# Kernel tuning notes

Hardware: AMD Instinct MI355X
Metric: run time of the kernel (lower is better)

The kernel has to match this reference:

```python
import jax, jax.numpy as jnp
import numpy as np

HEAD_SIZE = 128
N_EMBED = 2048
B, T = 4, 4096


def setup_inputs() -> dict:
    key = jax.random.key(0)
    kx, kq, kk, kv = jax.random.split(key, 4)
    s = 1.0 / np.sqrt(N_EMBED)
    return {
        "x": jax.random.normal(kx, (B, T, N_EMBED), dtype=jnp.float32),
        "Wq": jax.random.normal(kq, (N_EMBED, HEAD_SIZE), dtype=jnp.float32) * s,
        "Wk": jax.random.normal(kk, (N_EMBED, HEAD_SIZE), dtype=jnp.float32) * s,
        "Wv": jax.random.normal(kv, (N_EMBED, HEAD_SIZE), dtype=jnp.float32) * s,
    }


def reference(x, Wq, Wk, Wv):
    # x: [B, T, C]; projections (no bias)
    q = jnp.einsum('btc,cd->btd', x, Wq)  # [B, T, D]
    k = jnp.einsum('btc,cd->btd', x, Wk)
    v = jnp.einsum('btc,cd->btd', x, Wv)
    scale = q.shape[-1] ** -0.5
    scores = jnp.einsum('btd,bsd->bts', q, k) * scale  # [B, T, T]
    T_ = x.shape[1]
    causal = jnp.tril(jnp.ones((T_, T_), dtype=bool))
    scores = jnp.where(causal, scores, -jnp.inf)
    weight = jax.nn.softmax(scores, axis=-1)
    # dropout is identity in eval mode
    out = jnp.einsum('bts,bsd->btd', weight, v)  # [B, T, D]
    return out
```

## Files before the change

kernel.cpp:

```cpp
#include <hip/hip_runtime.h>
#include <hip/hip_bf16.h>
#include <stdint.h>

typedef unsigned short ushort_t;
typedef short v8s __attribute__((ext_vector_type(8)));
typedef float f32x4 __attribute__((ext_vector_type(4)));
typedef float f32x16 __attribute__((ext_vector_type(16)));

#define MFMA16(a, b, c) __builtin_amdgcn_mfma_f32_16x16x32_bf16(a, b, c, 0, 0, 0)
#define MFMA32(a, b, c) __builtin_amdgcn_mfma_f32_32x32x16_bf16(a, b, c, 0, 0, 0)

typedef __attribute__((address_space(1))) void gvoid;
typedef __attribute__((address_space(3))) void svoid;

__device__ __forceinline__ void gld16(const void* g, void* s) {
    __builtin_amdgcn_global_load_lds((gvoid*)g, (svoid*)s, 16, 0, 0);
}

__device__ __forceinline__ ushort_t f2bf(float f) {
    union { __hip_bfloat16 b; ushort_t u; } c;
    c.b = __float2bfloat16(f);
    return c.u;
}

__device__ __forceinline__ unsigned f2bf2(float a, float b) {
    union { __hip_bfloat162 b2; unsigned u; } c;
    c.b2 = __float22bfloat162_rn(make_float2(a, b));
    return c.u;
}

__global__ void transpose_w(const float* __restrict__ Wq, const float* __restrict__ Wk,
                            const float* __restrict__ Wv, ushort_t* __restrict__ WT) {
    __shared__ float tile[64][132];
    int bid = blockIdx.x;
    int w = bid >> 5;
    int k0 = (bid & 31) << 6;
    const float* W = (w == 0) ? Wq : ((w == 1) ? Wk : Wv);
    int tid = threadIdx.x;
    #pragma unroll
    for (int i = 0; i < 8; i++) {
        int row = i * 8 + (tid >> 5);
        int col = (tid & 31) * 4;
        float4 v = *(const float4*)(W + (size_t)(k0 + row) * 128 + col);
        tile[row][col] = v.x; tile[row][col + 1] = v.y;
        tile[row][col + 2] = v.z; tile[row][col + 3] = v.w;
    }
    __syncthreads();
    int n = tid >> 1, kh = (tid & 1) * 32;
    ushort_t* dst = WT + ((size_t)(w * 128 + n)) * 2048 + k0 + kh;
    #pragma unroll
    for (int j = 0; j < 32; j += 4) {
        union { ushort_t u[4]; uint2 v2; } pk;
        #pragma unroll
        for (int e = 0; e < 4; e++) pk.u[e] = f2bf(tile[kh + j + e][n]);
        *(uint2*)(dst + j) = pk.v2;
    }
}

#define PROJ_CVT_WRITE(RS, CUR)                                               \
    {                                                                         \
        union { unsigned u[4]; v8s v; } p0, p1;                               \
        p0.u[0] = f2bf2(RS[0][0], RS[0][1]); p0.u[1] = f2bf2(RS[0][2], RS[0][3]); \
        p0.u[2] = f2bf2(RS[1][0], RS[1][1]); p0.u[3] = f2bf2(RS[1][2], RS[1][3]); \
        p1.u[0] = f2bf2(RS[2][0], RS[2][1]); p1.u[1] = f2bf2(RS[2][2], RS[2][3]); \
        p1.u[2] = f2bf2(RS[3][0], RS[3][1]); p1.u[3] = f2bf2(RS[3][2], RS[3][3]); \
        *(v8s*)((char*)abuf + ((CUR) ^ 1) * 8192 + awb0) = p0.v;              \
        *(v8s*)((char*)abuf + ((CUR) ^ 1) * 8192 + awb1) = p1.v;              \
    }

#define PJ_STEP(IT, RLOAD, RCVT, DOX, DOB)                                    \
    {                                                                         \
        const int cur = (IT) & 1;                                             \
        if (DOB) {                                                            \
            _Pragma("unroll")                                                 \
            for (int i = 0; i < 6; i++)                                       \
                gld16(bsrc[i] + (size_t)((IT) + 1) * 128,                     \
                      (char*)bbuf + (cur ^ 1) * 24576 + (wid * 6 + i) * 1024);\
        }                                                                     \
        __builtin_amdgcn_sched_barrier(0);                                    \
        if (DOX) {                                                            \
            _Pragma("unroll")                                                 \
            for (int c = 0; c < 4; c++)                                       \
                RLOAD[c] = *(const f32x4*)(xp + (size_t)((IT) + 2) * 256 + c * 16); \
        }                                                                     \
        __builtin_amdgcn_sched_barrier(0);                                    \
        const char* ab = (const char*)abuf + cur * 8192;                      \
        const char* bb = (const char*)bbuf + cur * 24576;                     \
        _Pragma("unroll")                                                     \
        for (int kk = 0; kk < 2; kk++) {                                      \
            v8s af[4], bf[3];                                                 \
            _Pragma("unroll")                                                 \
            for (int m = 0; m < 4; m++) {                                     \
                int row = m * 16 + lr;                                        \
                af[m] = *(const v8s*)(ab + row * 128 +                        \
                         ((kk * 64 + lg * 16) ^ ((row & 7) << 4)));           \
            }                                                                 \
            _Pragma("unroll")                                                 \
            for (int n = 0; n < 3; n++) {                                     \
                int row = wid * 48 + n * 16 + lr;                             \
                bf[n] = *(const v8s*)(bb + row * 128 +                        \
                         ((kk * 64 + lg * 16) ^ ((row & 7) << 4)));           \
            }                                                                 \
            __builtin_amdgcn_s_setprio(1);                                    \
            _Pragma("unroll")                                                 \
            for (int m = 0; m < 4; m++)                                       \
                _Pragma("unroll")                                             \
                for (int n = 0; n < 3; n++)                                   \
                    acc[m][n] = MFMA16(af[m], bf[n], acc[m][n]);              \
            __builtin_amdgcn_s_setprio(0);                                    \
        }                                                                     \
        if (DOB) PROJ_CVT_WRITE(RCVT, cur);                                   \
        __builtin_amdgcn_sched_barrier(0);                                    \
        if (DOB) {                                                            \
            if (DOX) { asm volatile("s_waitcnt vmcnt(4)" ::: "memory"); }     \
            else     { asm volatile("s_waitcnt vmcnt(0)" ::: "memory"); }     \
            asm volatile("s_waitcnt lgkmcnt(0)" ::: "memory");                \
            __builtin_amdgcn_s_barrier();                                     \
        }                                                                     \
        __builtin_amdgcn_sched_barrier(0);                                    \
    }

__launch_bounds__(256, 2)
__global__ void proj_kernel(const float* __restrict__ x, const ushort_t* __restrict__ WT,
                            ushort_t* __restrict__ q, ushort_t* __restrict__ kb,
                            ushort_t* __restrict__ vb) {
    __shared__ ushort_t abuf[2][4096];
    __shared__ ushort_t bbuf[2][12288];

    int bid = blockIdx.x;
    int mt8 = bid & 7, nh = (bid >> 3) & 1, mg = bid >> 4;
    int mtile = mg * 8 + mt8;
    size_t m0 = (size_t)mtile * 64;
    int c0 = nh * 192;
    int tid = threadIdx.x, lane = tid & 63, wid = tid >> 6;
    int lg = lane >> 4, lr = lane & 15;

    f32x4 acc[4][3];
    #pragma unroll
    for (int m = 0; m < 4; m++)
        #pragma unroll
        for (int n = 0; n < 3; n++) acc[m][n] = (f32x4){0.f, 0.f, 0.f, 0.f};

    int ar = 16 * wid + (lane >> 2);
    const char* xp = (const char*)x + (m0 + ar) * 8192 + (lane & 3) * 64;
    int aswz = (ar & 7) << 4;
    int awb0 = ar * 128 + (((lane & 3) * 32 + 0) ^ aswz);
    int awb1 = ar * 128 + (((lane & 3) * 32 + 16) ^ aswz);

    const char* bsrc[6];
    #pragma unroll
    for (int i = 0; i < 6; i++) {
        int row = 8 * (wid * 6 + i) + (lane >> 3);
        int col = ((lane & 7) * 16) ^ ((row & 7) << 4);
        bsrc[i] = (const char*)WT + (size_t)(c0 + row) * 4096 + col;
    }

    f32x4 s0[4], s1[4];
    #pragma unroll
    for (int i = 0; i < 6; i++)
        gld16(bsrc[i], (char*)bbuf + (wid * 6 + i) * 1024);
    #pragma unroll
    for (int c = 0; c < 4; c++) s0[c] = *(const f32x4*)(xp + c * 16);
    #pragma unroll
    for (int c = 0; c < 4; c++) s1[c] = *(const f32x4*)(xp + 256 + c * 16);
    PROJ_CVT_WRITE(s0, 1);
    asm volatile("s_waitcnt lgkmcnt(0)" ::: "memory");
    __builtin_amdgcn_s_barrier();

    for (int it2 = 0; it2 < 30; it2 += 2) {
        PJ_STEP(it2,     s0, s1, 1, 1);
        PJ_STEP(it2 + 1, s1, s0, 1, 1);
    }
    PJ_STEP(30, s0, s1, 0, 1);
    PJ_STEP(31, s1, s0, 0, 0);

    #pragma unroll
    for (int m = 0; m < 4; m++) {
        #pragma unroll
        for (int e = 0; e < 4; e++) {
            size_t row = m0 + (size_t)(m * 16 + 4 * lg + e);
            int t = (int)(row & 4095);
            size_t base = (row >> 12) * 524288;
            #pragma unroll
            for (int n = 0; n < 3; n++) {
                int col = c0 + wid * 48 + n * 16 + lr;
                int w = col >> 7, d = col & 127;
                ushort_t val = f2bf(acc[m][n][e]);
                if (w == 0)
                    q[base + (size_t)(t >> 5) * 4096 + (d >> 4) * 512 + ((d >> 3) & 1) * 256 + (t & 31) * 8 + (d & 7)] = val;
                else if (w == 1)
                    kb[base + (size_t)(t >> 5) * 4096 + (d >> 4) * 512 + ((d >> 3) & 1) * 256 + (t & 31) * 8 + (d & 7)] = val;
                else
                    vb[base + (size_t)(t >> 4) * 2048 + (d >> 5) * 512 + ((t >> 3) & 1) * 256 + (d & 31) * 8 + (t & 7)] = val;
            }
        }
    }
}

__device__ __forceinline__ f32x16 zero16() {
    f32x16 z;
    #pragma unroll
    for (int i = 0; i < 16; i++) z[i] = 0.f;
    return z;
}

#define ATT_PVC(SV, BASE, VC, CNEXT)                                          \
    {                                                                         \
        unsigned a0 = f2bf2(SV[(BASE) + 0], SV[(BASE) + 1]);                  \
        unsigned a1 = f2bf2(SV[(BASE) + 2], SV[(BASE) + 3]);                  \
        unsigned b0 = f2bf2(SV[(BASE) + 4], SV[(BASE) + 5]);                  \
        unsigned b1 = f2bf2(SV[(BASE) + 6], SV[(BASE) + 7]);                  \
        unsigned snd0 = hi ? a0 : b0, snd1 = hi ? a1 : b1;                    \
        unsigned rcv0 = (unsigned)__shfl_xor((int)snd0, 32);                  \
        unsigned rcv1 = (unsigned)__shfl_xor((int)snd1, 32);                  \
        union { unsigned u[4]; v8s v; } pf;                                   \
        pf.u[0] = hi ? rcv0 : a0;                                             \
        pf.u[1] = hi ? rcv1 : a1;                                             \
        pf.u[2] = hi ? b0 : rcv0;                                             \
        pf.u[3] = hi ? b1 : rcv1;                                             \
        __builtin_amdgcn_s_setprio(1);                                        \
        _Pragma("unroll")                                                     \
        for (int dt = 0; dt < 4; dt++)                                        \
            accO[dt] = MFMA32(VC[dt], pf.v, accO[dt]);                        \
        __builtin_amdgcn_s_setprio(0);                                        \
        if ((CNEXT) >= 0) {                                                   \
            _Pragma("unroll")                                                 \
            for (int dt = 0; dt < 4; dt++)                                    \
                VC[dt] = *(const v8s*)(vg + (CNEXT) * 2048 + dt * 512);       \
        }                                                                     \
    }

__launch_bounds__(256, 2)
__global__ void attn_kernel(const ushort_t* __restrict__ q, const ushort_t* __restrict__ kb,
                            const ushort_t* __restrict__ vb, float* __restrict__ out) {
    __shared__ float obuf[4][4][16][64];
    __shared__ float stat[2][4][64];

    int bid = blockIdx.x;
    int xcd = bid & 7, rk = bid >> 3;
    int b = xcd >> 1;
    int g = rk * 2 + (xcd & 1);
    int qt = (g & 1) ? (g >> 1) : (127 - (g >> 1));
    int qt0 = qt * 32;
    int tid = threadIdx.x, lane = tid & 63, wid = tid >> 6;
    int hi = lane >> 5, lo = lane & 31;
    size_t bb = (size_t)b * 524288;
    int nt = (qt >> 1) + 1;
    const float cexp = 0.08838834764831845f * 1.4426950408889634f;

    v8s qf[8];
    {
        const ushort_t* qg = q + bb + (size_t)qt * 4096 + (size_t)lane * 8;
        #pragma unroll
        for (int ks = 0; ks < 8; ks++) qf[ks] = *(const v8s*)(qg + ks * 512);
    }

    f32x16 accO[4];
    #pragma unroll
    for (int dt = 0; dt < 4; dt++) accO[dt] = zero16();
    float mrun = -1e30f, lrun = 0.f;

    for (int t = wid; t < nt; t += 4) {
        const ushort_t* kg = kb + bb + (size_t)t * 8192 + (size_t)lane * 8;
        const ushort_t* vg = vb + bb + (size_t)t * 8192 + (size_t)lane * 8;

        f32x16 s0 = zero16(), s1 = zero16();
        __builtin_amdgcn_s_setprio(1);
        #pragma unroll
        for (int ks = 0; ks < 8; ks++) {
            v8s kf = *(const v8s*)(kg + ks * 512);
            s0 = MFMA32(kf, qf[ks], s0);
        }
        #pragma unroll
        for (int ks = 0; ks < 8; ks++) {
            v8s kf = *(const v8s*)(kg + 4096 + ks * 512);
            s1 = MFMA32(kf, qf[ks], s1);
        }
        __builtin_amdgcn_s_setprio(0);

        v8s vA[4], vB[4];
        #pragma unroll
        for (int dt = 0; dt < 4; dt++) vA[dt] = *(const v8s*)(vg + dt * 512);
        #pragma unroll
        for (int dt = 0; dt < 4; dt++) vB[dt] = *(const v8s*)(vg + 2048 + dt * 512);

        if (t == nt - 1) {
            int qrow = qt0 + lo;
            #pragma unroll
            for (int r = 0; r < 16; r++) {
                int kvb = t * 64 + (r & 3) + 8 * (r >> 2) + 4 * hi;
                if (kvb > qrow) s0[r] = -1e30f;
                if (kvb + 32 > qrow) s1[r] = -1e30f;
            }
        }

        float mx = s0[0];
        #pragma unroll
        for (int r = 1; r < 16; r++) mx = fmaxf(mx, s0[r]);
        #pragma unroll
        for (int r = 0; r < 16; r++) mx = fmaxf(mx, s1[r]);
        mx = fmaxf(mx, __shfl_xor(mx, 32));

        if (__any(mx > mrun + 62.7f)) {
            float mnew = fmaxf(mrun, mx);
            float fr = exp2f((mrun - mnew) * cexp);
            lrun *= fr;
            #pragma unroll
            for (int dt = 0; dt < 4; dt++)
                #pragma unroll
                for (int r = 0; r < 16; r++) accO[dt][r] *= fr;
            mrun = mnew;
        }
        float mc = mrun * cexp;
        float rs = 0.f;
        #pragma unroll
        for (int r = 0; r < 16; r++) { s0[r] = exp2f(fmaf(s0[r], cexp, -mc)); rs += s0[r]; }
        #pragma unroll
        for (int r = 0; r < 16; r++) { s1[r] = exp2f(fmaf(s1[r], cexp, -mc)); rs += s1[r]; }
        rs += __shfl_xor(rs, 32);
        lrun += rs;

        ATT_PVC(s0, 0, vA, 2);
        ATT_PVC(s0, 8, vB, 3);
        ATT_PVC(s1, 0, vA, -1);
        ATT_PVC(s1, 8, vB, -1);
    }

    #pragma unroll
    for (int dt = 0; dt < 4; dt++)
        #pragma unroll
        for (int r = 0; r < 16; r++)
            obuf[wid][dt][r][lane] = accO[dt][r];
    stat[0][wid][lane] = mrun;
    stat[1][wid][lane] = lrun;
    __syncthreads();

    float m0 = stat[0][0][lane], m1 = stat[0][1][lane];
    float m2 = stat[0][2][lane], m3 = stat[0][3][lane];
    float m = fmaxf(fmaxf(m0, m1), fmaxf(m2, m3));
    float f0 = exp2f((m0 - m) * cexp), f1 = exp2f((m1 - m) * cexp);
    float f2 = exp2f((m2 - m) * cexp), f3 = exp2f((m3 - m) * cexp);
    float lsum = f0 * stat[1][0][lane] + f1 * stat[1][1][lane]
               + f2 * stat[1][2][lane] + f3 * stat[1][3][lane];
    float linv = 1.0f / lsum;

    float o[16];
    #pragma unroll
    for (int r = 0; r < 16; r++)
        o[r] = (f0 * obuf[0][wid][r][lane] + f1 * obuf[1][wid][r][lane]
              + f2 * obuf[2][wid][r][lane] + f3 * obuf[3][wid][r][lane]) * linv;

    float* orow = out + ((size_t)b * 4096 + qt0 + lo) * 128 + wid * 32 + 4 * hi;
    #pragma unroll
    for (int a = 0; a < 4; a++) {
        float4 vv;
        vv.x = o[4 * a + 0]; vv.y = o[4 * a + 1];
        vv.z = o[4 * a + 2]; vv.w = o[4 * a + 3];
        *(float4*)(orow + 8 * a) = vv;
    }
}

extern "C" void kernel_launch(void* const* d_in, const int* in_sizes, int n_in,
                              void* d_out, int out_size, void* d_ws, size_t ws_size,
                              hipStream_t stream) {
    const float* x  = (const float*)d_in[0];
    const float* Wq = (const float*)d_in[1];
    const float* Wk = (const float*)d_in[2];
    const float* Wv = (const float*)d_in[3];
    float* out = (float*)d_out;
    char* ws = (char*)d_ws;

    ushort_t* q  = (ushort_t*)(ws);
    ushort_t* kb = (ushort_t*)(ws + (4u << 20));
    ushort_t* vb = (ushort_t*)(ws + (8u << 20));
    ushort_t* WT = (ushort_t*)(ws + (12u << 20));

    transpose_w<<<dim3(96), dim3(256), 0, stream>>>(Wq, Wk, Wv, WT);
    proj_kernel<<<dim3(512), dim3(256), 0, stream>>>(x, WT, q, kb, vb);
    attn_kernel<<<dim3(512), dim3(256), 0, stream>>>(q, kb, vb, out);
}
```

Before: 98.80 us.

## Retile projection kernel to 64x128 blocks with 2x2 waves and staggered K start

```diff
diff --git a/kernel.cpp b/kernel.cpp
--- a/kernel.cpp
+++ b/kernel.cpp
@@ -57,89 +57,91 @@
     }
 }
 
-#define PROJ_CVT_WRITE(RS, CUR)                                               \
+#define PJ_CVT_WRITE(RS, PAR)                                                 \
     {                                                                         \
         union { unsigned u[4]; v8s v; } p0, p1;                               \
         p0.u[0] = f2bf2(RS[0][0], RS[0][1]); p0.u[1] = f2bf2(RS[0][2], RS[0][3]); \
         p0.u[2] = f2bf2(RS[1][0], RS[1][1]); p0.u[3] = f2bf2(RS[1][2], RS[1][3]); \
         p1.u[0] = f2bf2(RS[2][0], RS[2][1]); p1.u[1] = f2bf2(RS[2][2], RS[2][3]); \
         p1.u[2] = f2bf2(RS[3][0], RS[3][1]); p1.u[3] = f2bf2(RS[3][2], RS[3][3]); \
-        *(v8s*)((char*)abuf + ((CUR) ^ 1) * 8192 + awb0) = p0.v;              \
-        *(v8s*)((char*)abuf + ((CUR) ^ 1) * 8192 + awb1) = p1.v;              \
-    }
-
-#define PJ_STEP(IT, RLOAD, RCVT, DOX, DOB)                                    \
+        *(v8s*)((char*)abuf + (PAR) * 8192 + awb0) = p0.v;                    \
+        *(v8s*)((char*)abuf + (PAR) * 8192 + awb1) = p1.v;                    \
+    }
+
+#define PJ_STEP(PAR, J, RLOAD, RCVT, DOX, DOB)                                \
     {                                                                         \
-        const int cur = (IT) & 1;                                             \
         if (DOB) {                                                            \
-            _Pragma("unroll")                                                 \
-            for (int i = 0; i < 6; i++)                                       \
-                gld16(bsrc[i] + (size_t)((IT) + 1) * 128,                     \
-                      (char*)bbuf + (cur ^ 1) * 24576 + (wid * 6 + i) * 1024);\
+            int itn = (koff + (J) + 1) & 31;                                  \
+            _Pragma("unroll")                                                 \
+            for (int i = 0; i < 4; i++)                                       \
+                gld16(bsrc[i] + (size_t)itn * 128,                            \
+                      (char*)bbuf + ((PAR) ^ 1) * 16384 + (4 * wid + i) * 1024); \
         }                                                                     \
         __builtin_amdgcn_sched_barrier(0);                                    \
         if (DOX) {                                                            \
+            int itx = (koff + (J) + 2) & 31;                                  \
             _Pragma("unroll")                                                 \
             for (int c = 0; c < 4; c++)                                       \
-                RLOAD[c] = *(const f32x4*)(xp + (size_t)((IT) + 2) * 256 + c * 16); \
+                RLOAD[c] = *(const f32x4*)(xp + (size_t)itx * 256 + c * 16);  \
         }                                                                     \
         __builtin_amdgcn_sched_barrier(0);                                    \
-        const char* ab = (const char*)abuf + cur * 8192;                      \
-        const char* bb = (const char*)bbuf + cur * 24576;                     \
+        const char* ab = (const char*)abuf + (PAR) * 8192;                    \
+        const char* bb = (const char*)bbuf + (PAR) * 16384;                   \
         _Pragma("unroll")                                                     \
         for (int kk = 0; kk < 2; kk++) {                                      \
-            v8s af[4], bf[3];                                                 \
-            _Pragma("unroll")                                                 \
-            for (int m = 0; m < 4; m++) {                                     \
-                int row = m * 16 + lr;                                        \
+            v8s af[2], bf[4];                                                 \
+            _Pragma("unroll")                                                 \
+            for (int m = 0; m < 2; m++) {                                     \
+                int row = wr * 32 + m * 16 + lr;                              \
                 af[m] = *(const v8s*)(ab + row * 128 +                        \
                          ((kk * 64 + lg * 16) ^ ((row & 7) << 4)));           \
             }                                                                 \
             _Pragma("unroll")                                                 \
-            for (int n = 0; n < 3; n++) {                                     \
-                int row = wid * 48 + n * 16 + lr;                             \
+            for (int n = 0; n < 4; n++) {                                     \
+                int row = wc * 64 + n * 16 + lr;                              \
                 bf[n] = *(const v8s*)(bb + row * 128 +                        \
                          ((kk * 64 + lg * 16) ^ ((row & 7) << 4)));           \
             }                                                                 \
             __builtin_amdgcn_s_setprio(1);                                    \
             _Pragma("unroll")                                                 \
-            for (int m = 0; m < 4; m++)                                       \
+            for (int m = 0; m < 2; m++)                                       \
                 _Pragma("unroll")                                             \
-                for (int n = 0; n < 3; n++)                                   \
+                for (int n = 0; n < 4; n++)                                   \
                     acc[m][n] = MFMA16(af[m], bf[n], acc[m][n]);              \
             __builtin_amdgcn_s_setprio(0);                                    \
         }                                                                     \
-        if (DOB) PROJ_CVT_WRITE(RCVT, cur);                                   \
-        __builtin_amdgcn_sched_barrier(0);                                    \
         if (DOB) {                                                            \
+            PJ_CVT_WRITE(RCVT, (PAR) ^ 1);                                    \
             if (DOX) { asm volatile("s_waitcnt vmcnt(4)" ::: "memory"); }     \
             else     { asm volatile("s_waitcnt vmcnt(0)" ::: "memory"); }     \
             asm volatile("s_waitcnt lgkmcnt(0)" ::: "memory");                \
             __builtin_amdgcn_s_barrier();                                     \
         }                                                                     \
-        __builtin_amdgcn_sched_barrier(0);                                    \
-    }
-
-__launch_bounds__(256, 2)
+    }
+
+__launch_bounds__(256, 3)
 __global__ void proj_kernel(const float* __restrict__ x, const ushort_t* __restrict__ WT,
                             ushort_t* __restrict__ q, ushort_t* __restrict__ kb,
                             ushort_t* __restrict__ vb) {
     __shared__ ushort_t abuf[2][4096];
-    __shared__ ushort_t bbuf[2][12288];
+    __shared__ ushort_t bbuf[2][8192];
 
     int bid = blockIdx.x;
-    int mt8 = bid & 7, nh = (bid >> 3) & 1, mg = bid >> 4;
-    int mtile = mg * 8 + mt8;
+    int xcd = bid & 7, idx = bid >> 3;
+    int mt_local = idx / 3, ng = idx - 3 * mt_local;
+    int mtile = xcd * 32 + mt_local;
     size_t m0 = (size_t)mtile * 64;
-    int c0 = nh * 192;
+    int c0 = ng * 128;
+    int koff = ((bid >> 8) * 11) & 31;
     int tid = threadIdx.x, lane = tid & 63, wid = tid >> 6;
     int lg = lane >> 4, lr = lane & 15;
-
-    f32x4 acc[4][3];
-    #pragma unroll
-    for (int m = 0; m < 4; m++)
-        #pragma unroll
-        for (int n = 0; n < 3; n++) acc[m][n] = (f32x4){0.f, 0.f, 0.f, 0.f};
+    int wr = wid >> 1, wc = wid & 1;
+
+    f32x4 acc[2][4];
+    #pragma unroll
+    for (int m = 0; m < 2; m++)
+        #pragma unroll
+        for (int n = 0; n < 4; n++) acc[m][n] = (f32x4){0.f, 0.f, 0.f, 0.f};
 
     int ar = 16 * wid + (lane >> 2);
     const char* xp = (const char*)x + (m0 + ar) * 8192 + (lane & 3) * 64;
@@ -147,48 +149,51 @@
     int awb0 = ar * 128 + (((lane & 3) * 32 + 0) ^ aswz);
     int awb1 = ar * 128 + (((lane & 3) * 32 + 16) ^ aswz);
 
-    const char* bsrc[6];
-    #pragma unroll
-    for (int i = 0; i < 6; i++) {
-        int row = 8 * (wid * 6 + i) + (lane >> 3);
+    const char* bsrc[4];
+    #pragma unroll
+    for (int i = 0; i < 4; i++) {
+        int row = 8 * (4 * wid + i) + (lane >> 3);
         int col = ((lane & 7) * 16) ^ ((row & 7) << 4);
         bsrc[i] = (const char*)WT + (size_t)(c0 + row) * 4096 + col;
     }
 
-    f32x4 s0[4], s1[4];
-    #pragma unroll
-    for (int i = 0; i < 6; i++)
-        gld16(bsrc[i], (char*)bbuf + (wid * 6 + i) * 1024);
-    #pragma unroll
-    for (int c = 0; c < 4; c++) s0[c] = *(const f32x4*)(xp + c * 16);
-    #pragma unroll
-    for (int c = 0; c < 4; c++) s1[c] = *(const f32x4*)(xp + 256 + c * 16);
-    PROJ_CVT_WRITE(s0, 1);
-    asm volatile("s_waitcnt lgkmcnt(0)" ::: "memory");
-    __builtin_amdgcn_s_barrier();
-
-    for (int it2 = 0; it2 < 30; it2 += 2) {
-        PJ_STEP(it2,     s0, s1, 1, 1);
-        PJ_STEP(it2 + 1, s1, s0, 1, 1);
-    }
-    PJ_STEP(30, s0, s1, 0, 1);
-    PJ_STEP(31, s1, s0, 0, 0);
-
-    #pragma unroll
-    for (int m = 0; m < 4; m++) {
+    f32x4 xs0[4], xs1[4];
+    {
+        int it0 = koff, it1 = (koff + 1) & 31;
+        #pragma unroll
+        for (int i = 0; i < 4; i++)
+            gld16(bsrc[i] + (size_t)it0 * 128, (char*)bbuf + (4 * wid + i) * 1024);
+        #pragma unroll
+        for (int c = 0; c < 4; c++) xs0[c] = *(const f32x4*)(xp + (size_t)it0 * 256 + c * 16);
+        #pragma unroll
+        for (int c = 0; c < 4; c++) xs1[c] = *(const f32x4*)(xp + (size_t)it1 * 256 + c * 16);
+        PJ_CVT_WRITE(xs0, 0);
+        asm volatile("s_waitcnt vmcnt(0)" ::: "memory");
+        asm volatile("s_waitcnt lgkmcnt(0)" ::: "memory");
+        __builtin_amdgcn_s_barrier();
+    }
+
+    for (int j = 0; j < 30; j += 2) {
+        PJ_STEP(0, j,     xs0, xs1, 1, 1);
+        PJ_STEP(1, j + 1, xs1, xs0, 1, 1);
+    }
+    PJ_STEP(0, 30, xs0, xs1, 0, 1);
+    PJ_STEP(1, 31, xs1, xs0, 0, 0);
+
+    #pragma unroll
+    for (int m = 0; m < 2; m++) {
         #pragma unroll
         for (int e = 0; e < 4; e++) {
-            size_t row = m0 + (size_t)(m * 16 + 4 * lg + e);
+            size_t row = m0 + (size_t)(wr * 32 + m * 16 + 4 * lg + e);
             int t = (int)(row & 4095);
             size_t base = (row >> 12) * 524288;
             #pragma unroll
-            for (int n = 0; n < 3; n++) {
-                int col = c0 + wid * 48 + n * 16 + lr;
-                int w = col >> 7, d = col & 127;
+            for (int n = 0; n < 4; n++) {
+                int d = (wc * 64 + n * 16 + lr) & 127;
                 ushort_t val = f2bf(acc[m][n][e]);
-                if (w == 0)
+                if (ng == 0)
                     q[base + (size_t)(t >> 5) * 4096 + (d >> 4) * 512 + ((d >> 3) & 1) * 256 + (t & 31) * 8 + (d & 7)] = val;
-                else if (w == 1)
+                else if (ng == 1)
                     kb[base + (size_t)(t >> 5) * 4096 + (d >> 4) * 512 + ((d >> 3) & 1) * 256 + (t & 31) * 8 + (d & 7)] = val;
                 else
                     vb[base + (size_t)(t >> 4) * 2048 + (d >> 5) * 512 + ((t >> 3) & 1) * 256 + (d & 31) * 8 + (t & 7)] = val;
@@ -376,6 +381,6 @@
     ushort_t* WT = (ushort_t*)(ws + (12u << 20));
 
     transpose_w<<<dim3(96), dim3(256), 0, stream>>>(Wq, Wk, Wv, WT);
-    proj_kernel<<<dim3(512), dim3(256), 0, stream>>>(x, WT, q, kb, vb);
+    proj_kernel<<<dim3(768), dim3(256), 0, stream>>>(x, WT, q, kb, vb);
     attn_kernel<<<dim3(512), dim3(256), 0, stream>>>(q, kb, vb, out);
 }
```

Measured after the change: 104.4 us. +5.7%, slower.
